# Performance work log

Hardware: AMD Instinct MI355X
Metric: run time of the kernel (lower is better)

## Reference

```python
import jax, jax.numpy as jnp
import numpy as np
from jax import lax

EPS_BN = 1e-5
SMOOTH = 1e-5


def conv3x3(x, w):
    # x: [N,C,H,W], w: [O,I,3,3], stride 1, padding 1 (SAME)
    return lax.conv_general_dilated(
        x, w, window_strides=(1, 1), padding='SAME',
        dimension_numbers=('NCHW', 'OIHW', 'NCHW'))


def batchnorm(x, gamma, beta):
    # training-mode BatchNorm2d: batch statistics over (N,H,W), biased var
    mean = jnp.mean(x, axis=(0, 2, 3), keepdims=True)
    var = jnp.mean(jnp.square(x - mean), axis=(0, 2, 3), keepdims=True)
    g = gamma.reshape(1, -1, 1, 1)
    b = beta.reshape(1, -1, 1, 1)
    return (x - mean) * lax.rsqrt(var + EPS_BN) * g + b


def tanimoto(a, b, axes):
    tpl = jnp.sum(a * b, axis=axes, keepdims=True)
    sq = jnp.sum(a * a + b * b, axis=axes, keepdims=True)
    return (tpl + SMOOTH) / (sq - tpl + SMOOTH)


def tanimoto_compl(a, b, axes):
    return 0.5 * (tanimoto(a, b, axes) + tanimoto(1.0 - a, 1.0 - b, axes))


def setup_inputs() -> dict:
    key = jax.random.key(0)
    ks = jax.random.split(key, 5)
    N, Cin, Cout, H, W = 8, 64, 64, 256, 256
    x = jax.random.normal(ks[0], (N, Cin, H, W), dtype=jnp.float32)
    fan = Cin * 9
    wq = jax.random.normal(ks[1], (Cout, Cin, 3, 3), dtype=jnp.float32) / np.sqrt(fan)
    wk = jax.random.normal(ks[2], (Cout, Cin, 3, 3), dtype=jnp.float32) / np.sqrt(fan)
    wv = jax.random.normal(ks[3], (Cout, Cin, 3, 3), dtype=jnp.float32) / np.sqrt(fan)
    ones = jnp.ones((Cout,), dtype=jnp.float32)
    zeros = jnp.zeros((Cout,), dtype=jnp.float32)
    return {
        'x': x,
        'wq': wq, 'gq': ones, 'bq': zeros,
        'wk': wk, 'gk': ones, 'bk': zeros,
        'wv': wv, 'gv': ones, 'bv': zeros,
        'g_norm': ones, 'b_norm': zeros,
    }


def reference(x, wq, gq, bq, wk, gk, bk, wv, gv, bv, g_norm, b_norm):
    q = jax.nn.sigmoid(batchnorm(conv3x3(x, wq), gq, bq))
    k = jax.nn.sigmoid(batchnorm(conv3x3(x, wk), gk, bk))
    v = jax.nn.sigmoid(batchnorm(conv3x3(x, wv), gv, bv))
    attn_spatial = tanimoto_compl(q, k, axes=(1,))      # [N,1,H,W]
    attn_channel = tanimoto_compl(q, k, axes=(2, 3))    # [N,C,1,1]
    attention = 0.5 * (attn_spatial * v + attn_channel * v)
    return batchnorm(attention, g_norm, b_norm)
```

## Files before the change

### kernel.cpp

```cpp
#include <hip/hip_runtime.h>

typedef unsigned short u16;
typedef __attribute__((ext_vector_type(8))) short short8;
typedef __attribute__((ext_vector_type(4))) float f32x4;
typedef __attribute__((ext_vector_type(16))) float f32x16;

#define OFF_SUMS 0ul
#define OFF_WT   26624ul
#define OFF_ASP  247808ul
#define OFF_CONV 2344960ul
#define S_SUM   0
#define S_SSQ   768
#define S_SC    1536
#define S_BI    1728
#define M_A1    1920
#define M_A23   2432
#define M_A45   2944
#define M_V1    3456
#define M_V2    3968
#define M_AV    4480
#define M_AV2   4992
#define M_A2V2  5504
#define S_ACH   6016
#define S_SCA   6528
#define S_BIA   6592
#define S_NFLOAT 6656

__device__ __forceinline__ float bf2f(u16 v) {
  union { unsigned u; float f; } x; x.u = ((unsigned)v) << 16; return x.f;
}
__device__ __forceinline__ u16 f2bf(float f) {
  union { float f; unsigned u; } x; x.f = f;
  unsigned r = x.u + 0x7fffu + ((x.u >> 16) & 1u);
  return (u16)(r >> 16);
}
__device__ __forceinline__ float frcp(float x) { return __builtin_amdgcn_rcpf(x); }
__device__ __forceinline__ float sigmoidf_(float x) { return frcp(1.f + __expf(-x)); }

template <int CTRL, int RMASK>
__device__ __forceinline__ float dpp_add(float x) {
  int m = __builtin_amdgcn_update_dpp(0, __builtin_bit_cast(int, x), CTRL, RMASK, 0xf, true);
  return x + __builtin_bit_cast(float, m);
}
__device__ __forceinline__ float wsum64(float x) {
  x = dpp_add<0x111, 0xf>(x);
  x = dpp_add<0x112, 0xf>(x);
  x = dpp_add<0x114, 0xf>(x);
  x = dpp_add<0x118, 0xf>(x);
  x = dpp_add<0x142, 0xa>(x);
  x = dpp_add<0x143, 0xc>(x);
  return __builtin_bit_cast(float, __builtin_amdgcn_readlane(__builtin_bit_cast(int, x), 63));
}

__global__ void transpose_k(const float* __restrict__ x, u16* __restrict__ xt) {
  __shared__ u16 t[64][130];
  const int bid = blockIdx.x;
  const int wtile = bid & 1, h = (bid >> 1) & 255, n = bid >> 9;
  const int w0 = wtile << 7;
  const int tid = threadIdx.x;
  for (int i = tid; i < 8192; i += 256) {
    int c = i >> 7, w = i & 127;
    t[c][w] = f2bf(x[(((n << 6) + c) << 16) + (h << 8) + w0 + w]);
  }
  __syncthreads();
  for (int i = tid; i < 8192; i += 256) {
    int w = i >> 6, c = i & 63;
    xt[(long)((((n << 8) + h) << 8) + w0 + w) * 64 + c] = t[c][w];
  }
}

__global__ void repack_k(const float* __restrict__ wq, const float* __restrict__ wk,
                         const float* __restrict__ wv, u16* __restrict__ wt) {
  int i = blockIdx.x * 256 + threadIdx.x;
  if (i >= 110592) return;
  int j = i & 7, l = (i >> 3) & 63, kc = (i >> 9) & 3;
  int t2 = i >> 11;
  int ocg = t2 % 6, dydx = t2 / 6;
  int oc = ocg * 32 + (l & 31);
  int ch = kc * 16 + (l >> 5) * 8 + j;
  int cs = oc >> 6, ol = oc & 63;
  const float* src = cs == 0 ? wq : (cs == 1 ? wk : wv);
  wt[i] = f2bf(src[(ol * 64 + ch) * 9 + dydx]);
}

__global__ __launch_bounds__(256, 2) void conv_k(const u16* __restrict__ xt,
                                                 const u16* __restrict__ wt,
                                                 u16* __restrict__ conv,
                                                 float* __restrict__ S) {
  __shared__ u16 lx[3 * 8320];
  const int bid = blockIdx.x;
  const int wtile = bid & 1, h = (bid >> 1) & 255, n = bid >> 9;
  const int w0 = wtile << 7;
  const int tid = threadIdx.x;
  for (int g = tid; g < 3120; g += 256) {
    int row = g / 1040;
    int r2 = g - row * 1040;
    int w = r2 >> 3, cg = r2 & 7;
    int hs = h + row - 1, wsr = w0 + w - 1;
    uint4 val = make_uint4(0u, 0u, 0u, 0u);
    if ((unsigned)hs < 256u && (unsigned)wsr < 256u)
      val = *(const uint4*)(xt + (long)((((n << 8) + hs) << 8) + wsr) * 64 + (cg << 3));
    int idx = ((w << 6) + (cg << 3)) ^ ((w & 7) << 3);
    *(uint4*)(&lx[row * 8320 + idx]) = val;
  }
  __syncthreads();
  const int lane = tid & 63, wave = tid >> 6;
  const int l31 = lane & 31, half = lane >> 5;
  const int wm = wave & 1, wn = wave >> 1;
  f32x16 acc[3][2];
#pragma unroll
  for (int a = 0; a < 3; ++a)
#pragma unroll
    for (int b = 0; b < 2; ++b)
#pragma unroll
      for (int e = 0; e < 16; ++e) acc[a][b][e] = 0.f;

#pragma unroll
  for (int dy = 0; dy < 3; ++dy) {
#pragma unroll
    for (int dx = 0; dx < 3; ++dx) {
      const u16* wp = wt + (dy * 3 + dx) * 12288;
      short8 bfr[3][4];
#pragma unroll
      for (int nt = 0; nt < 3; ++nt)
#pragma unroll
        for (int kc = 0; kc < 4; ++kc)
          bfr[nt][kc] = *(const short8*)(wp + ((wn * 3 + nt) * 4 + kc) * 512 + lane * 8);
#pragma unroll
      for (int kc = 0; kc < 4; ++kc) {
        short8 afr[2];
#pragma unroll
        for (int mt = 0; mt < 2; ++mt) {
          const int px = wm * 64 + mt * 32 + l31 + dx;
          const int chb = kc * 16 + half * 8;
          int idx = ((px << 6) + chb) ^ ((px & 7) << 3);
          afr[mt] = *(const short8*)(&lx[dy * 8320 + idx]);
        }
#pragma unroll
        for (int mt = 0; mt < 2; ++mt)
#pragma unroll
          for (int nt = 0; nt < 3; ++nt)
            acc[nt][mt] = __builtin_amdgcn_mfma_f32_32x32x16_bf16(afr[mt], bfr[nt][kc], acc[nt][mt], 0, 0, 0);
      }
    }
  }
  const long pix0 = (long)bid * 128 + wm * 64;
#pragma unroll
  for (int nt = 0; nt < 3; ++nt) {
    const int oc = wn * 96 + nt * 32 + l31;
#pragma unroll
    for (int mt = 0; mt < 2; ++mt) {
      const long pxb = pix0 + mt * 32 + half * 4;
#pragma unroll
      for (int rq = 0; rq < 4; ++rq)
#pragma unroll
        for (int rr = 0; rr < 4; ++rr) {
          const long px = pxb + rr + 8 * rq;
          conv[px * 192 + oc] = f2bf(acc[nt][mt][rq * 4 + rr]);
        }
    }
  }
  const int sh = (bid & 3) * 192;
#pragma unroll
  for (int nt = 0; nt < 3; ++nt) {
    float s = 0.f, ss = 0.f;
#pragma unroll
    for (int mt = 0; mt < 2; ++mt)
#pragma unroll
      for (int r = 0; r < 16; ++r) {
        float x = acc[nt][mt][r];
        s += x; ss += x * x;
      }
    s += __shfl_xor(s, 32); ss += __shfl_xor(ss, 32);
    if (lane < 32) {
      const int oc = wn * 96 + nt * 32 + lane;
      atomicAdd(&S[S_SUM + sh + oc], s);
      atomicAdd(&S[S_SSQ + sh + oc], ss);
    }
  }
}

__global__ void bnparam_k(float* __restrict__ S, const float* gq, const float* bq, const float* gk,
                          const float* bk, const float* gv, const float* bv) {
  int t = threadIdx.x;
  int cv = t >> 6, c = t & 63;
  float g = cv == 0 ? gq[c] : (cv == 1 ? gk[c] : gv[c]);
  float b = cv == 0 ? bq[c] : (cv == 1 ? bk[c] : bv[c]);
  float sm = 0.f, sq = 0.f;
#pragma unroll
  for (int sh = 0; sh < 4; ++sh) { sm += S[S_SUM + sh * 192 + t]; sq += S[S_SSQ + sh * 192 + t]; }
  const float inv = 1.f / 524288.f;
  float mean = sm * inv;
  float var = sq * inv - mean * mean;
  float rstd = rsqrtf(var + 1e-5f);
  float sc = g * rstd;
  S[S_SC + t] = sc;
  S[S_BI + t] = b - mean * sc;
}

__global__ void k3_k(const u16* __restrict__ conv, float* __restrict__ S, float* __restrict__ asp) {
  __shared__ float red[4][8][64];
  const int tid = threadIdx.x, lane = tid & 63, wave = tid >> 6;
  const int bid = blockIdx.x;
  const int n = bid >> 9;
  const long p0 = (long)bid * 128 + wave * 32;
  const float sq = S[S_SC + lane], bq = S[S_BI + lane];
  const float sk = S[S_SC + 64 + lane], bk = S[S_BI + 64 + lane];
  const float sv = S[S_SC + 128 + lane], bv = S[S_BI + 128 + lane];
  float A1 = 0.f, A23 = 0.f, A45 = 0.f, V1 = 0.f, V2 = 0.f, AV = 0.f, AV2 = 0.f, A2V2 = 0.f;
  float myasp = 0.f;
#pragma unroll 4
  for (int i = 0; i < 32; ++i) {
    const u16* row = conv + (p0 + i) * 192;
    float q = sigmoidf_(bf2f(row[lane]) * sq + bq);
    float k = sigmoidf_(bf2f(row[64 + lane]) * sk + bk);
    float v = sigmoidf_(bf2f(row[128 + lane]) * sv + bv);
    float p1 = q * k, p23 = q * q + k * k, p45 = q + k;
    A1 += p1; A23 += p23; A45 += p45;
    float s1 = wsum64(p1);
    float s23 = wsum64(p23);
    float s45 = wsum64(p45);
    const float sm = 1e-5f;
    float t1 = (s1 + sm) * frcp(s23 - s1 + sm);
    float t2 = (64.f - s45 + s1 + sm) * frcp(64.f - s45 + s23 - s1 + sm);
    float a = 0.5f * (t1 + t2);
    if (i == (lane & 31)) myasp = a;
    float av = a * v;
    V1 += v; V2 += v * v; AV += av; AV2 += av * v; A2V2 += av * av;
  }
  if (lane < 32) asp[p0 + lane] = myasp;
  red[wave][0][lane] = A1;  red[wave][1][lane] = A23; red[wave][2][lane] = A45;
  red[wave][3][lane] = V1;  red[wave][4][lane] = V2;  red[wave][5][lane] = AV;
  red[wave][6][lane] = AV2; red[wave][7][lane] = A2V2;
  __syncthreads();
  if (tid < 64) {
    const int mb[8] = {M_A1, M_A23, M_A45, M_V1, M_V2, M_AV, M_AV2, M_A2V2};
#pragma unroll
    for (int m = 0; m < 8; ++m) {
      float t = red[0][m][tid] + red[1][m][tid] + red[2][m][tid] + red[3][m][tid];
      atomicAdd(&S[mb[m] + n * 64 + tid], t);
    }
  }
}

__global__ void k4_k(float* __restrict__ S, const float* gn, const float* bn_) {
  __shared__ float r1[512], r2[512];
  const int t = threadIdx.x;
  float A1 = S[M_A1 + t], A23 = S[M_A23 + t], A45 = S[M_A45 + t];
  const float sm = 1e-5f, cnt = 65536.f;
  float t1 = (A1 + sm) / (A23 - A1 + sm);
  float t2 = (cnt - A45 + A1 + sm) / (cnt - A45 + A23 - A1 + sm);
  float ach = 0.5f * (t1 + t2);
  S[S_ACH + t] = ach;
  r1[t] = 0.5f * (S[M_AV + t] + ach * S[M_V1 + t]);
  r2[t] = 0.25f * (S[M_A2V2 + t] + 2.f * ach * S[M_AV2 + t] + ach * ach * S[M_V2 + t]);
  __syncthreads();
  if (t < 64) {
    float s = 0.f, ss = 0.f;
#pragma unroll
    for (int n = 0; n < 8; ++n) { s += r1[n * 64 + t]; ss += r2[n * 64 + t]; }
    const float inv = 1.f / 524288.f;
    float mean = s * inv;
    float var = ss * inv - mean * mean;
    float rstd = rsqrtf(var + 1e-5f);
    float sc = gn[t] * rstd;
    S[S_SCA + t] = sc;
    S[S_BIA + t] = bn_[t] - mean * sc;
  }
}

__global__ void k6_k(const u16* __restrict__ conv, const float* __restrict__ S,
                     const float* __restrict__ asp, float* __restrict__ out) {
  __shared__ float t[128][65];
  const int tid = threadIdx.x, lane = tid & 63, wave = tid >> 6;
  const int n = blockIdx.x >> 9;
  const int hw0 = (blockIdx.x & 511) << 7;
  const long P0 = (long)blockIdx.x * 128;
  const float sv = S[S_SC + 128 + lane], bv = S[S_BI + 128 + lane];
  const float av = S[S_ACH + n * 64 + lane];
  const float sA = S[S_SCA + lane], bA = S[S_BIA + lane];
  for (int i = wave; i < 128; i += 4) {
    const long p = P0 + i;
    float v = sigmoidf_(bf2f(conv[p * 192 + 128 + lane]) * sv + bv);
    float att = 0.5f * (asp[p] + av) * v;
    t[i][lane] = att * sA + bA;
  }
  __syncthreads();
  const int c = tid >> 2, sub = tid & 3;
  const long plane = ((long)((n << 6) + c)) << 16;
  for (int i = 0; i < 8; ++i) {
    const int pst = (i * 4 + sub) << 2;
    f32x4 vbuf;
#pragma unroll
    for (int j = 0; j < 4; ++j) vbuf[j] = t[pst + j][c];
    *(f32x4*)(&out[plane + hw0 + pst]) = vbuf;
  }
}

extern "C" void kernel_launch(void* const* d_in, const int* in_sizes, int n_in,
                              void* d_out, int out_size, void* d_ws, size_t ws_size,
                              hipStream_t stream) {
  (void)in_sizes; (void)n_in; (void)out_size; (void)ws_size;
  const float* x  = (const float*)d_in[0];
  const float* wq = (const float*)d_in[1];
  const float* gq = (const float*)d_in[2];
  const float* bq = (const float*)d_in[3];
  const float* wk = (const float*)d_in[4];
  const float* gk = (const float*)d_in[5];
  const float* bk = (const float*)d_in[6];
  const float* wv = (const float*)d_in[7];
  const float* gv = (const float*)d_in[8];
  const float* bv = (const float*)d_in[9];
  const float* gn = (const float*)d_in[10];
  const float* bn_ = (const float*)d_in[11];
  char* ws = (char*)d_ws;
  float* S   = (float*)(ws + OFF_SUMS);
  u16* wt    = (u16*)(ws + OFF_WT);
  float* asp = (float*)(ws + OFF_ASP);
  u16* conv  = (u16*)(ws + OFF_CONV);
  float* out = (float*)d_out;
  u16* xt  = (u16*)d_out;

  (void)hipMemsetAsync(S, 0, S_NFLOAT * 4, stream);
  transpose_k<<<4096, 256, 0, stream>>>(x, xt);
  repack_k<<<432, 256, 0, stream>>>(wq, wk, wv, wt);
  conv_k<<<4096, 256, 0, stream>>>(xt, wt, conv, S);
  bnparam_k<<<1, 192, 0, stream>>>(S, gq, bq, gk, bk, gv, bv);
  k3_k<<<4096, 256, 0, stream>>>(conv, S, asp);
  k4_k<<<1, 512, 0, stream>>>(S, gn, bn_);
  k6_k<<<4096, 256, 0, stream>>>(conv, S, asp, out);
}
```

Baseline: 552.6 us.

## Fold tiny BN-param kernels into consumers and vectorize transpose

Merges the weight repack into the transpose launch, removes the single-block bnparam and k4 kernels by recomputing BN scale/bias per block inside k3 and k6, and vectorizes the transpose's global loads/stores (f32x4 reads, uint4 writes). This cuts three launches and their serialization gaps and widens memory accesses. In exchange every block redundantly re-reads the stats and recomputes the parameters, and k6 does an 8-iteration reduction with divisions per block.

```diff
diff --git a/kernel.cpp b/kernel.cpp
--- a/kernel.cpp
+++ b/kernel.cpp
@@ -11,8 +11,6 @@
 #define OFF_CONV 2344960ul
 #define S_SUM   0
 #define S_SSQ   768
-#define S_SC    1536
-#define S_BI    1728
 #define M_A1    1920
 #define M_A23   2432
 #define M_A45   2944
@@ -21,9 +19,6 @@
 #define M_AV    4480
 #define M_AV2   4992
 #define M_A2V2  5504
-#define S_ACH   6016
-#define S_SCA   6528
-#define S_BIA   6592
 #define S_NFLOAT 6656
 
 __device__ __forceinline__ float bf2f(u16 v) {
@@ -52,35 +47,52 @@
   return __builtin_bit_cast(float, __builtin_amdgcn_readlane(__builtin_bit_cast(int, x), 63));
 }
 
-__global__ void transpose_k(const float* __restrict__ x, u16* __restrict__ xt) {
+__global__ void tr_k(const float* __restrict__ x, u16* __restrict__ xt,
+                     const float* __restrict__ wq, const float* __restrict__ wk,
+                     const float* __restrict__ wv, u16* __restrict__ wt) {
+  const int bid = blockIdx.x;
+  const int tid = threadIdx.x;
+  if (bid >= 4096) {
+    int i = (bid - 4096) * 256 + tid;
+    if (i >= 110592) return;
+    int j = i & 7, l = (i >> 3) & 63, kc = (i >> 9) & 3;
+    int t2 = i >> 11;
+    int ocg = t2 % 6, dydx = t2 / 6;
+    int oc = ocg * 32 + (l & 31);
+    int ch = kc * 16 + (l >> 5) * 8 + j;
+    int cs = oc >> 6, ol = oc & 63;
+    const float* src = cs == 0 ? wq : (cs == 1 ? wk : wv);
+    wt[i] = f2bf(src[(ol * 64 + ch) * 9 + dydx]);
+    return;
+  }
   __shared__ u16 t[64][130];
-  const int bid = blockIdx.x;
   const int wtile = bid & 1, h = (bid >> 1) & 255, n = bid >> 9;
   const int w0 = wtile << 7;
-  const int tid = threadIdx.x;
-  for (int i = tid; i < 8192; i += 256) {
-    int c = i >> 7, w = i & 127;
-    t[c][w] = f2bf(x[(((n << 6) + c) << 16) + (h << 8) + w0 + w]);
-  }
-  __syncthreads();
-  for (int i = tid; i < 8192; i += 256) {
-    int w = i >> 6, c = i & 63;
-    xt[(long)((((n << 8) + h) << 8) + w0 + w) * 64 + c] = t[c][w];
-  }
-}
-
-__global__ void repack_k(const float* __restrict__ wq, const float* __restrict__ wk,
-                         const float* __restrict__ wv, u16* __restrict__ wt) {
-  int i = blockIdx.x * 256 + threadIdx.x;
-  if (i >= 110592) return;
-  int j = i & 7, l = (i >> 3) & 63, kc = (i >> 9) & 3;
-  int t2 = i >> 11;
-  int ocg = t2 % 6, dydx = t2 / 6;
-  int oc = ocg * 32 + (l & 31);
-  int ch = kc * 16 + (l >> 5) * 8 + j;
-  int cs = oc >> 6, ol = oc & 63;
-  const float* src = cs == 0 ? wq : (cs == 1 ? wk : wv);
-  wt[i] = f2bf(src[(ol * 64 + ch) * 9 + dydx]);
+#pragma unroll
+  for (int it = 0; it < 8; ++it) {
+    int i = it * 256 + tid;
+    int c = i >> 5, w4 = (i & 31) << 2;
+    const f32x4 v = *(const f32x4*)(&x[(((long)((n << 6) + c)) << 16) + (h << 8) + w0 + w4]);
+    unsigned p0 = (unsigned)f2bf(v[0]) | ((unsigned)f2bf(v[1]) << 16);
+    unsigned p1 = (unsigned)f2bf(v[2]) | ((unsigned)f2bf(v[3]) << 16);
+    *(unsigned*)(&t[c][w4]) = p0;
+    *(unsigned*)(&t[c][w4 + 2]) = p1;
+  }
+  __syncthreads();
+#pragma unroll
+  for (int it = 0; it < 4; ++it) {
+    int i = it * 256 + tid;
+    int c8 = (i & 7) << 3, w = i >> 3;
+    unsigned short u[8];
+#pragma unroll
+    for (int j = 0; j < 8; ++j) u[j] = t[c8 + j][w];
+    uint4 val;
+    val.x = (unsigned)u[0] | ((unsigned)u[1] << 16);
+    val.y = (unsigned)u[2] | ((unsigned)u[3] << 16);
+    val.z = (unsigned)u[4] | ((unsigned)u[5] << 16);
+    val.w = (unsigned)u[6] | ((unsigned)u[7] << 16);
+    *(uint4*)(xt + (long)((((n << 8) + h) << 8) + w0 + w) * 64 + c8) = val;
+  }
 }
 
 __global__ __launch_bounds__(256, 2) void conv_k(const u16* __restrict__ xt,
@@ -180,41 +192,43 @@
   }
 }
 
-__global__ void bnparam_k(float* __restrict__ S, const float* gq, const float* bq, const float* gk,
-                          const float* bk, const float* gv, const float* bv) {
-  int t = threadIdx.x;
-  int cv = t >> 6, c = t & 63;
-  float g = cv == 0 ? gq[c] : (cv == 1 ? gk[c] : gv[c]);
-  float b = cv == 0 ? bq[c] : (cv == 1 ? bk[c] : bv[c]);
-  float sm = 0.f, sq = 0.f;
-#pragma unroll
-  for (int sh = 0; sh < 4; ++sh) { sm += S[S_SUM + sh * 192 + t]; sq += S[S_SSQ + sh * 192 + t]; }
-  const float inv = 1.f / 524288.f;
-  float mean = sm * inv;
-  float var = sq * inv - mean * mean;
-  float rstd = rsqrtf(var + 1e-5f);
-  float sc = g * rstd;
-  S[S_SC + t] = sc;
-  S[S_BI + t] = b - mean * sc;
-}
-
-__global__ void k3_k(const u16* __restrict__ conv, float* __restrict__ S, float* __restrict__ asp) {
+__global__ void k3_k(const u16* __restrict__ conv, float* __restrict__ S, float* __restrict__ asp,
+                     const float* __restrict__ gq, const float* __restrict__ bq,
+                     const float* __restrict__ gk, const float* __restrict__ bk,
+                     const float* __restrict__ gv, const float* __restrict__ bv) {
   __shared__ float red[4][8][64];
+  __shared__ float scb[192], bib[192];
   const int tid = threadIdx.x, lane = tid & 63, wave = tid >> 6;
   const int bid = blockIdx.x;
   const int n = bid >> 9;
   const long p0 = (long)bid * 128 + wave * 32;
-  const float sq = S[S_SC + lane], bq = S[S_BI + lane];
-  const float sk = S[S_SC + 64 + lane], bk = S[S_BI + 64 + lane];
-  const float sv = S[S_SC + 128 + lane], bv = S[S_BI + 128 + lane];
+  if (tid < 192) {
+    int cv = tid >> 6, c = tid & 63;
+    float g = cv == 0 ? gq[c] : (cv == 1 ? gk[c] : gv[c]);
+    float b = cv == 0 ? bq[c] : (cv == 1 ? bk[c] : bv[c]);
+    float sm = 0.f, sq2 = 0.f;
+#pragma unroll
+    for (int sh = 0; sh < 4; ++sh) { sm += S[S_SUM + sh * 192 + tid]; sq2 += S[S_SSQ + sh * 192 + tid]; }
+    const float inv = 1.f / 524288.f;
+    float mean = sm * inv;
+    float var = sq2 * inv - mean * mean;
+    float rstd = rsqrtf(var + 1e-5f);
+    float sc = g * rstd;
+    scb[tid] = sc;
+    bib[tid] = b - mean * sc;
+  }
+  __syncthreads();
+  const float sq = scb[lane], bq_ = bib[lane];
+  const float sk = scb[64 + lane], bk_ = bib[64 + lane];
+  const float sv = scb[128 + lane], bv_ = bib[128 + lane];
   float A1 = 0.f, A23 = 0.f, A45 = 0.f, V1 = 0.f, V2 = 0.f, AV = 0.f, AV2 = 0.f, A2V2 = 0.f;
   float myasp = 0.f;
 #pragma unroll 4
   for (int i = 0; i < 32; ++i) {
     const u16* row = conv + (p0 + i) * 192;
-    float q = sigmoidf_(bf2f(row[lane]) * sq + bq);
-    float k = sigmoidf_(bf2f(row[64 + lane]) * sk + bk);
-    float v = sigmoidf_(bf2f(row[128 + lane]) * sv + bv);
+    float q = sigmoidf_(bf2f(row[lane]) * sq + bq_);
+    float k = sigmoidf_(bf2f(row[64 + lane]) * sk + bk_);
+    float v = sigmoidf_(bf2f(row[128 + lane]) * sv + bv_);
     float p1 = q * k, p23 = q * q + k * k, p45 = q + k;
     A1 += p1; A23 += p23; A45 += p45;
     float s1 = wsum64(p1);
@@ -243,45 +257,58 @@
   }
 }
 
-__global__ void k4_k(float* __restrict__ S, const float* gn, const float* bn_) {
-  __shared__ float r1[512], r2[512];
-  const int t = threadIdx.x;
-  float A1 = S[M_A1 + t], A23 = S[M_A23 + t], A45 = S[M_A45 + t];
-  const float sm = 1e-5f, cnt = 65536.f;
-  float t1 = (A1 + sm) / (A23 - A1 + sm);
-  float t2 = (cnt - A45 + A1 + sm) / (cnt - A45 + A23 - A1 + sm);
-  float ach = 0.5f * (t1 + t2);
-  S[S_ACH + t] = ach;
-  r1[t] = 0.5f * (S[M_AV + t] + ach * S[M_V1 + t]);
-  r2[t] = 0.25f * (S[M_A2V2 + t] + 2.f * ach * S[M_AV2 + t] + ach * ach * S[M_V2 + t]);
-  __syncthreads();
-  if (t < 64) {
-    float s = 0.f, ss = 0.f;
-#pragma unroll
-    for (int n = 0; n < 8; ++n) { s += r1[n * 64 + t]; ss += r2[n * 64 + t]; }
-    const float inv = 1.f / 524288.f;
-    float mean = s * inv;
-    float var = ss * inv - mean * mean;
-    float rstd = rsqrtf(var + 1e-5f);
-    float sc = gn[t] * rstd;
-    S[S_SCA + t] = sc;
-    S[S_BIA + t] = bn_[t] - mean * sc;
-  }
-}
-
 __global__ void k6_k(const u16* __restrict__ conv, const float* __restrict__ S,
-                     const float* __restrict__ asp, float* __restrict__ out) {
+                     const float* __restrict__ asp, float* __restrict__ out,
+                     const float* __restrict__ gv, const float* __restrict__ bv,
+                     const float* __restrict__ gn, const float* __restrict__ bn_) {
   __shared__ float t[128][65];
+  __shared__ float svv[64], bvv[64], achb[64], sAv[64], bAv[64];
   const int tid = threadIdx.x, lane = tid & 63, wave = tid >> 6;
   const int n = blockIdx.x >> 9;
   const int hw0 = (blockIdx.x & 511) << 7;
   const long P0 = (long)blockIdx.x * 128;
-  const float sv = S[S_SC + 128 + lane], bv = S[S_BI + 128 + lane];
-  const float av = S[S_ACH + n * 64 + lane];
-  const float sA = S[S_SCA + lane], bA = S[S_BIA + lane];
+  if (tid < 64) {
+    const float inv = 1.f / 524288.f;
+    float sm = 0.f, sq2 = 0.f;
+#pragma unroll
+    for (int sh = 0; sh < 4; ++sh) {
+      sm += S[S_SUM + sh * 192 + 128 + tid];
+      sq2 += S[S_SSQ + sh * 192 + 128 + tid];
+    }
+    float mean = sm * inv;
+    float var = sq2 * inv - mean * mean;
+    float rstd = rsqrtf(var + 1e-5f);
+    float sv = gv[tid] * rstd;
+    svv[tid] = sv;
+    bvv[tid] = bv[tid] - mean * sv;
+    const float smc = 1e-5f, cnt = 65536.f;
+    float s1 = 0.f, s2 = 0.f, myach = 0.f;
+#pragma unroll
+    for (int nn = 0; nn < 8; ++nn) {
+      int idx = nn * 64 + tid;
+      float A1 = S[M_A1 + idx], A23 = S[M_A23 + idx], A45 = S[M_A45 + idx];
+      float t1 = (A1 + smc) / (A23 - A1 + smc);
+      float t2 = (cnt - A45 + A1 + smc) / (cnt - A45 + A23 - A1 + smc);
+      float ach = 0.5f * (t1 + t2);
+      if (nn == n) myach = ach;
+      s1 += 0.5f * (S[M_AV + idx] + ach * S[M_V1 + idx]);
+      s2 += 0.25f * (S[M_A2V2 + idx] + 2.f * ach * S[M_AV2 + idx] + ach * ach * S[M_V2 + idx]);
+    }
+    float mean2 = s1 * inv;
+    float var2 = s2 * inv - mean2 * mean2;
+    float rstd2 = rsqrtf(var2 + 1e-5f);
+    float sA = gn[tid] * rstd2;
+    sAv[tid] = sA;
+    bAv[tid] = bn_[tid] - mean2 * sA;
+    achb[tid] = myach;
+  }
+  __syncthreads();
+  const float sv = svv[lane], bvx = bvv[lane];
+  const float av = achb[lane];
+  const float sA = sAv[lane], bA = bAv[lane];
   for (int i = wave; i < 128; i += 4) {
     const long p = P0 + i;
-    float v = sigmoidf_(bf2f(conv[p * 192 + 128 + lane]) * sv + bv);
+    float v = sigmoidf_(bf2f(conv[p * 192 + 128 + lane]) * sv + bvx);
     float att = 0.5f * (asp[p] + av) * v;
     t[i][lane] = att * sA + bA;
   }
@@ -322,11 +349,8 @@
   u16* xt  = (u16*)d_out;
 
   (void)hipMemsetAsync(S, 0, S_NFLOAT * 4, stream);
-  transpose_k<<<4096, 256, 0, stream>>>(x, xt);
-  repack_k<<<432, 256, 0, stream>>>(wq, wk, wv, wt);
+  tr_k<<<4528, 256, 0, stream>>>(x, xt, wq, wk, wv, wt);
   conv_k<<<4096, 256, 0, stream>>>(xt, wt, conv, S);
-  bnparam_k<<<1, 192, 0, stream>>>(S, gq, bq, gk, bk, gv, bv);
-  k3_k<<<4096, 256, 0, stream>>>(conv, S, asp);
-  k4_k<<<1, 512, 0, stream>>>(S, gn, bn_);
-  k6_k<<<4096, 256, 0, stream>>>(conv, S, asp, out);
-}
+  k3_k<<<4096, 256, 0, stream>>>(conv, S, asp, gq, bq, gk, bk, gv, bv);
+  k6_k<<<4096, 256, 0, stream>>>(conv, S, asp, out, gv, bv, gn, bn_);
+}
```

New measurement: 551.2 us. No clear change (-0.2%).
